# Kernel optimization log

Hardware: AMD Instinct MI355X
Metric: run time of the kernel (lower is better)

Reference implementation:

```python
import jax, jax.numpy as jnp
import numpy as np

B, L, C, D = 8, 2048, 64, 32
N = 16
LENGTH = 64  # max block length (exclusive upper bound per original np.random.randint(length-1)+1)


def setup_inputs() -> dict:
    key = jax.random.key(0)
    kx, ks, kl, kc = jax.random.split(key, 4)
    x = jax.random.normal(kx, (B, L, C, D), dtype=jnp.float32)
    starts = jax.random.randint(ks, (N,), 0, L, dtype=jnp.int32)
    # original: l = np.random.randint(length - 1) + 1  -> l in [1, length-1]
    lengths = jax.random.randint(kl, (N,), 1, LENGTH, dtype=jnp.int32)
    channels = jax.random.randint(kc, (N,), 0, C, dtype=jnp.int32)
    return {"x": x, "starts": starts, "lengths": lengths, "channels": channels}


def reference(x, starts, lengths, channels):
    # x: [B, L, C, D]; zero x[:, start:start+l, chan, :] for each of N blocks.
    t = jnp.arange(x.shape[1], dtype=starts.dtype)  # [L]
    covered = (t[None, :] >= starts[:, None]) & (t[None, :] < starts[:, None] + lengths[:, None])  # [N, L]
    chan_onehot = jax.nn.one_hot(channels, x.shape[2], dtype=jnp.bool_)  # [N, C]
    zeroed = jnp.any(covered[:, :, None] & chan_onehot[:, None, :], axis=0)  # [L, C]
    keep = jnp.where(zeroed, jnp.float32(0), jnp.float32(1))  # [L, C]
    return x * keep[None, :, :, None]
```

## Files before the change

kernel.cpp:

```cpp
#include <hip/hip_runtime.h>


#define BB 8
#define LL 2048
#define CC 64
#define DD 32
#define NBLK 16

__global__ __launch_bounds__(256) void masking_kernel(
    const float4* __restrict__ x,
    const int* __restrict__ starts,
    const int* __restrict__ lengths,
    const int* __restrict__ channels,
    float4* __restrict__ out,
    int n4)
{
    int st[NBLK], en[NBLK], ch[NBLK];
#pragma unroll
    for (int n = 0; n < NBLK; ++n) {
        st[n] = starts[n];
        en[n] = st[n] + lengths[n];
        ch[n] = channels[n];
    }

    const int stride = gridDim.x * blockDim.x;
    for (int i = blockIdx.x * blockDim.x + threadIdx.x; i < n4; i += stride) {
        const int lc = i >> 3;
        const int c  = lc & (CC - 1);
        const int l  = (lc >> 6) & (LL - 1);

        bool z = false;
#pragma unroll
        for (int n = 0; n < NBLK; ++n) {
            z |= (c == ch[n]) & (l >= st[n]) & (l < en[n]);
        }
        const float m = z ? 0.0f : 1.0f;

        float4 v = x[i];
        v.x *= m; v.y *= m; v.z *= m; v.w *= m;
        out[i] = v;
    }
}

extern "C" void kernel_launch(void* const* d_in, const int* in_sizes, int n_in,
                              void* d_out, int out_size, void* d_ws, size_t ws_size,
                              hipStream_t stream)
{
    const float4* x      = (const float4*)d_in[0];
    const int* starts    = (const int*)d_in[1];
    const int* lengths   = (const int*)d_in[2];
    const int* channels  = (const int*)d_in[3];
    float4* out          = (float4*)d_out;

    const int n4 = (BB * LL * CC * DD) / 4;
    const int threads = 256;
    const int blocks = 2048;

    masking_kernel<<<blocks, threads, 0, stream>>>(x, starts, lengths, channels, out, n4);
}
```

Baseline: 50.39 us.

## Compute mask once per (l,c) and reuse across batch with nontemporal stores

Replaces the grid-stride loop with one thread per (l, c, d4) position. Each thread computes the mask once and applies it to all 8 batch elements, issuing the 8 loads together before the stores. Stores use nontemporal hints to reduce cache pollution. This removes redundant mask evaluation and gives more memory-level parallelism per thread, in exchange for more registers and a fixed grid sized to the problem.

```diff
diff --git a/kernel.cpp b/kernel.cpp
--- a/kernel.cpp
+++ b/kernel.cpp
@@ -7,13 +7,14 @@
 #define DD 32
 #define NBLK 16
 
+typedef float v4f __attribute__((ext_vector_type(4)));
+
 __global__ __launch_bounds__(256) void masking_kernel(
-    const float4* __restrict__ x,
+    const v4f* __restrict__ x,
     const int* __restrict__ starts,
     const int* __restrict__ lengths,
     const int* __restrict__ channels,
-    float4* __restrict__ out,
-    int n4)
+    v4f* __restrict__ out)
 {
     int st[NBLK], en[NBLK], ch[NBLK];
 #pragma unroll
@@ -23,22 +24,28 @@
         ch[n] = channels[n];
     }
 
-    const int stride = gridDim.x * blockDim.x;
-    for (int i = blockIdx.x * blockDim.x + threadIdx.x; i < n4; i += stride) {
-        const int lc = i >> 3;
-        const int c  = lc & (CC - 1);
-        const int l  = (lc >> 6) & (LL - 1);
+    const int tid = blockIdx.x * blockDim.x + threadIdx.x;
+    const int STRIDE = LL * CC * (DD / 4);
 
-        bool z = false;
+    const int lc = tid >> 3;
+    const int c  = lc & (CC - 1);
+    const int l  = lc >> 6;
+
+    bool z = false;
 #pragma unroll
-        for (int n = 0; n < NBLK; ++n) {
-            z |= (c == ch[n]) & (l >= st[n]) & (l < en[n]);
-        }
-        const float m = z ? 0.0f : 1.0f;
+    for (int n = 0; n < NBLK; ++n) {
+        z |= (c == ch[n]) & (l >= st[n]) & (l < en[n]);
+    }
+    const float m = z ? 0.0f : 1.0f;
 
-        float4 v = x[i];
-        v.x *= m; v.y *= m; v.z *= m; v.w *= m;
-        out[i] = v;
+    v4f v[BB];
+#pragma unroll
+    for (int b = 0; b < BB; ++b) {
+        v[b] = x[tid + b * STRIDE];
+    }
+#pragma unroll
+    for (int b = 0; b < BB; ++b) {
+        __builtin_nontemporal_store(v[b] * m, &out[tid + b * STRIDE]);
     }
 }
 
@@ -46,15 +53,14 @@
                               void* d_out, int out_size, void* d_ws, size_t ws_size,
                               hipStream_t stream)
 {
-    const float4* x      = (const float4*)d_in[0];
+    const v4f* x         = (const v4f*)d_in[0];
     const int* starts    = (const int*)d_in[1];
     const int* lengths   = (const int*)d_in[2];
     const int* channels  = (const int*)d_in[3];
-    float4* out          = (float4*)d_out;
+    v4f* out             = (v4f*)d_out;
 
-    const int n4 = (BB * LL * CC * DD) / 4;
     const int threads = 256;
-    const int blocks = 2048;
+    const int blocks  = (LL * CC * (DD / 4)) / threads;
 
-    masking_kernel<<<blocks, threads, 0, stream>>>(x, starts, lengths, channels, out, n4);
+    masking_kernel<<<blocks, threads, 0, stream>>>(x, starts, lengths, channels, out);
 }
```

Result: faster. 45.72 us (-9.3%).
